# Kernel optimization log

Hardware: AMD Instinct MI355X
Metric: run time of the kernel (lower is better)

Reference implementation:

```python
import jax, jax.numpy as jnp
import numpy as np

INPUT_BINS = (100, 200, 500, 1000, 5000, 20000, 73200)  # sum = 100000
BATCH = 512


def setup_inputs() -> dict:
    key = jax.random.key(0)
    k1, k2, k3 = jax.random.split(key, 3)
    total = sum(INPUT_BINS)
    logits = jax.random.normal(k1, (BATCH, total), dtype=jnp.float32)
    # min(INPUT_BINS) == 100, so targets in [0, 100) are valid for every column
    targets = jax.random.randint(k2, (BATCH, len(INPUT_BINS)), 0, 100, dtype=jnp.int32)
    mask = jax.random.randint(k3, (BATCH, total), 0, 2, dtype=jnp.int32).astype(bool)
    return {
        "targets": targets,
        "logits": logits,
        "mask": mask,
        "input_bins": INPUT_BINS,
        "nb_negative": 1000,
        "n_samples": 20,
    }


def reference(targets, logits, mask, input_bins, nb_negative, n_samples):
    B = targets.shape[0]
    recon = jnp.zeros((B,), dtype=logits.dtype)
    sample_key = jax.random.key(42)
    start = 0
    for i, nb in enumerate(input_bins):  # loop over fixed small column set (7)
        sl = logits[:, start:start + nb]          # [B, nb]
        obs = ~mask[:, start:start + nb]          # [B, nb] observed entries
        t = targets[:, i].astype(jnp.int32)       # [B]
        if nb <= nb_negative:
            # c_logits = log_softmax(slice); nll on (c_logits * obs) at target idx
            logp = jax.nn.log_softmax(sl, axis=1) * obs.astype(sl.dtype)
            recon = recon - jnp.take_along_axis(logp, t[:, None], axis=1)[:, 0]
        else:
            # multinomial over uniform observed probs == categorical over
            # logits that are 0 where observed, -inf where masked
            sample_key, sk = jax.random.split(sample_key)
            samp_dist = jnp.where(obs, 0.0, -jnp.inf).astype(jnp.float32)
            neg = jax.random.categorical(sk, samp_dist, axis=-1,
                                         shape=(n_samples, B)).T  # [B, n_samples]
            rs = jnp.concatenate([t[:, None], neg.astype(jnp.int32)], axis=1)  # [B, 1+n_samples]
            sampled = jnp.take_along_axis(sl, rs, axis=1)
            # cross_entropy with soft target [1,0,...,0] == -log_softmax(...)[:, 0]
            recon = recon - jax.nn.log_softmax(sampled, axis=1)[:, 0]
        start += nb
    loss = recon.sum()
    avg_loss = recon.sum() / (B * np.log(2))
    return (loss, avg_loss)
```

## Files before the change

### kernel.cpp

```cpp
#include <hip/hip_runtime.h>
#include <stdint.h>

#define BATCH 512
#define NBINS 7
#define TOTAL 100000

__device__ __constant__ int c_off[NBINS] = {0, 100, 300, 800, 1800, 6800, 26800};
__device__ __constant__ int c_nb[NBINS]  = {100, 200, 500, 1000, 5000, 20000, 73200};

__device__ __forceinline__ uint64_t mix64(uint64_t z) {
    z += 0x9E3779B97F4A7C15ULL;
    z = (z ^ (z >> 30)) * 0xBF58476D1CE4E5B9ULL;
    z = (z ^ (z >> 27)) * 0x94D049BB133111EBULL;
    return z ^ (z >> 31);
}

__global__ __launch_bounds__(512) void row_kernel(const float* __restrict__ logits,
                                                  const int* __restrict__ targets,
                                                  const int* __restrict__ mask,
                                                  float* __restrict__ row_loss) {
    int b = blockIdx.x;
    int tid = threadIdx.x;
    int wave = tid >> 6;
    int lane = tid & 63;

    __shared__ float terms[7];

    if (wave < 4) {
        int off = c_off[wave], nb = c_nb[wave];
        const float* row = logits + (size_t)b * TOTAL + off;
        const float4* r4 = (const float4*)row;
        int n4 = nb >> 2;

        float m_l = -INFINITY, s_l = 0.f;
        for (int j = lane; j < n4; j += 64) {
            float4 v = r4[j];
            float mv = fmaxf(fmaxf(v.x, v.y), fmaxf(v.z, v.w));
            float mn = fmaxf(m_l, mv);
            s_l = s_l * expf(m_l - mn)
                + expf(v.x - mn) + expf(v.y - mn) + expf(v.z - mn) + expf(v.w - mn);
            m_l = mn;
        }
        float m = m_l;
        for (int k = 32; k; k >>= 1) m = fmaxf(m, __shfl_xor(m, k));
        float c = s_l * expf(m_l - m);
        for (int k = 32; k; k >>= 1) c += __shfl_xor(c, k);

        if (lane == 0) {
            float lse = m + logf(c);
            int t = targets[b * NBINS + wave];
            bool obs_t = (mask[(size_t)b * TOTAL + off + t] == 0);
            terms[wave] = obs_t ? (lse - row[t]) : 0.f;
        }
    } else if (wave < 7) {
        int bin = wave;
        int off = c_off[bin], nb = c_nb[bin];
        const float* row = logits + (size_t)b * TOTAL + off;
        const int* mrow = mask + (size_t)b * TOTAL + off;

        int t = targets[b * NBINS + bin];
        float tv = row[t];

        int task = b * 3 + (bin - 4);
        float m_l = -INFINITY, s_l = 0.f;
        int have = 0;
        for (int r = 0; r < 4 && have < 20; ++r) {
            uint64_t h = mix64(((uint64_t)task << 20) | ((uint64_t)r << 6) | (uint64_t)lane);
            int pos = (int)(((h >> 32) * (uint64_t)nb) >> 32);
            bool obs = (mrow[pos] == 0);
            unsigned long long bal = __ballot(obs);
            int cnt = __popcll(bal);
            int take = min(cnt, 20 - have);
            int j = __popcll(bal & ((1ULL << lane) - 1ULL));
            if (obs && j < take) {
                float v = row[pos];
                float mn = fmaxf(m_l, v);
                s_l = s_l * expf(m_l - mn) + expf(v - mn);
                m_l = mn;
            }
            have += take;
        }
        float m = fmaxf(m_l, tv);
        for (int k = 32; k; k >>= 1) m = fmaxf(m, __shfl_xor(m, k));
        float c = s_l * expf(m_l - m);
        for (int k = 32; k; k >>= 1) c += __shfl_xor(c, k);

        if (lane == 0) terms[bin] = m + logf(c + expf(tv - m)) - tv;
    }

    __syncthreads();
    if (tid == 0) {
        row_loss[b] = terms[0] + terms[1] + terms[2] + terms[3]
                    + terms[4] + terms[5] + terms[6];
    }
}

__global__ void reduce_kernel(const float* __restrict__ row_loss,
                              float* __restrict__ out) {
    int lane = threadIdx.x;
    float s = 0.f;
    for (int j = lane; j < BATCH; j += 64) s += row_loss[j];
    for (int k = 32; k; k >>= 1) s += __shfl_xor(s, k);
    if (lane == 0) {
        out[0] = s;
        out[1] = s / (512.0f * 0.69314718055994530942f);
    }
}

extern "C" void kernel_launch(void* const* d_in, const int* in_sizes, int n_in,
                              void* d_out, int out_size, void* d_ws, size_t ws_size,
                              hipStream_t stream) {
    const int*   targets = (const int*)d_in[0];
    const float* logits  = (const float*)d_in[1];
    const int*   mask    = (const int*)d_in[2];

    float* row_loss = (float*)d_ws;
    float* out = (float*)d_out;

    row_kernel<<<BATCH, 512, 0, stream>>>(logits, targets, mask, row_loss);
    reduce_kernel<<<1, 64, 0, stream>>>(row_loss, out);
}
```

Before: 11.92 us.

## Fuse final reduction into row kernel via fixed-point atomics and last-block finish

Removes the separate reduce kernel. Each block adds its row loss, converted to fixed point, into a 64-bit atomic accumulator, and the last block to arrive (tracked by an atomic counter) writes both outputs. A memset clears the accumulator and counter on every launch. Separately, the sampled-bin loop now loads the logit alongside the mask word instead of after the ballot, so the two loads can overlap. The memset is itself a stream operation, so it partly offsets the launch saved. The fixed-point scale also limits precision and range, and negative row losses would wrap under the unsigned cast.

Measured after the change: 25.58 us. 115% more time.

```diff
diff --git a/kernel.cpp b/kernel.cpp
--- a/kernel.cpp
+++ b/kernel.cpp
@@ -4,6 +4,7 @@
 #define BATCH 512
 #define NBINS 7
 #define TOTAL 100000
+#define FXSCALE 16777216.0f
 
 __device__ __constant__ int c_off[NBINS] = {0, 100, 300, 800, 1800, 6800, 26800};
 __device__ __constant__ int c_nb[NBINS]  = {100, 200, 500, 1000, 5000, 20000, 73200};
@@ -15,10 +16,12 @@
     return z ^ (z >> 31);
 }
 
-__global__ __launch_bounds__(512) void row_kernel(const float* __restrict__ logits,
-                                                  const int* __restrict__ targets,
-                                                  const int* __restrict__ mask,
-                                                  float* __restrict__ row_loss) {
+__global__ __launch_bounds__(512) void fused_row_kernel(const float* __restrict__ logits,
+                                                        const int* __restrict__ targets,
+                                                        const int* __restrict__ mask,
+                                                        unsigned long long* __restrict__ acc,
+                                                        unsigned int* __restrict__ ctr,
+                                                        float* __restrict__ out) {
     int b = blockIdx.x;
     int tid = threadIdx.x;
     int wave = tid >> 6;
@@ -67,13 +70,14 @@
         for (int r = 0; r < 4 && have < 20; ++r) {
             uint64_t h = mix64(((uint64_t)task << 20) | ((uint64_t)r << 6) | (uint64_t)lane);
             int pos = (int)(((h >> 32) * (uint64_t)nb) >> 32);
-            bool obs = (mrow[pos] == 0);
+            int mk = mrow[pos];
+            float v = row[pos];
+            bool obs = (mk == 0);
             unsigned long long bal = __ballot(obs);
             int cnt = __popcll(bal);
             int take = min(cnt, 20 - have);
             int j = __popcll(bal & ((1ULL << lane) - 1ULL));
             if (obs && j < take) {
-                float v = row[pos];
                 float mn = fmaxf(m_l, v);
                 s_l = s_l * expf(m_l - mn) + expf(v - mn);
                 m_l = mn;
@@ -90,20 +94,19 @@
 
     __syncthreads();
     if (tid == 0) {
-        row_loss[b] = terms[0] + terms[1] + terms[2] + terms[3]
-                    + terms[4] + terms[5] + terms[6];
-    }
-}
-
-__global__ void reduce_kernel(const float* __restrict__ row_loss,
-                              float* __restrict__ out) {
-    int lane = threadIdx.x;
-    float s = 0.f;
-    for (int j = lane; j < BATCH; j += 64) s += row_loss[j];
-    for (int k = 32; k; k >>= 1) s += __shfl_xor(s, k);
-    if (lane == 0) {
-        out[0] = s;
-        out[1] = s / (512.0f * 0.69314718055994530942f);
+        float rl = terms[0] + terms[1] + terms[2] + terms[3]
+                 + terms[4] + terms[5] + terms[6];
+        unsigned long long s = (unsigned long long)llrintf(rl * FXSCALE);
+        atomicAdd(acc, s);
+        __threadfence();
+        unsigned int old = atomicAdd(ctr, 1u);
+        if (old == BATCH - 1) {
+            __threadfence();
+            unsigned long long tot = atomicAdd(acc, 0ULL);
+            float loss = (float)((double)tot / (double)FXSCALE);
+            out[0] = loss;
+            out[1] = loss / (512.0f * 0.69314718055994530942f);
+        }
     }
 }
 
@@ -114,9 +117,11 @@
     const float* logits  = (const float*)d_in[1];
     const int*   mask    = (const int*)d_in[2];
 
-    float* row_loss = (float*)d_ws;
+    unsigned long long* acc = (unsigned long long*)d_ws;
+    unsigned int*       ctr = (unsigned int*)((char*)d_ws + 8);
     float* out = (float*)d_out;
 
-    row_kernel<<<BATCH, 512, 0, stream>>>(logits, targets, mask, row_loss);
-    reduce_kernel<<<1, 64, 0, stream>>>(row_loss, out);
+    hipMemsetAsync(d_ws, 0, 16, stream);
+
+    fused_row_kernel<<<BATCH, 512, 0, stream>>>(logits, targets, mask, acc, ctr, out);
 }
```
